# Performance work log

Hardware: AMD Instinct MI355X
Metric: run time of the kernel (lower is better)

Reference implementation:

```python
import jax, jax.numpy as jnp
import numpy as np

IN_FEATURES = 4096
OUT_FEATURES = 11008


def setup_inputs() -> dict:
    key = jax.random.key(0)
    kx, kw, ks, kb = jax.random.split(key, 4)
    x = jax.random.normal(kx, (64, IN_FEATURES), dtype=jnp.float32)
    # int8 quantized weight, stored as int32 for portability (values in [-128, 127])
    weight_quantized = jax.random.randint(kw, (OUT_FEATURES, IN_FEATURES), -128, 128, dtype=jnp.int32)
    # per-tensor scale, as produced by quantize_weights_int8: |w|.max()/127
    weight_scale = jnp.asarray(0.01, dtype=jnp.float32)
    bias = jax.random.normal(kb, (OUT_FEATURES,), dtype=jnp.float32) * 0.02
    return {"x": x, "weight_quantized": weight_quantized, "weight_scale": weight_scale, "bias": bias}


def reference(x, weight_quantized, weight_scale, bias):
    # dequantize_weights_int8: q.float() * scale, then F.linear(x, W, b) = x @ W.T + b
    weight = weight_quantized.astype(jnp.float32) * weight_scale  # [out, in]
    return jnp.einsum('mi,oi->mo', x, weight) + bias
```

## Files before the change

kernel.cpp:

```cpp
#include <hip/hip_runtime.h>
#include <hip/hip_bf16.h>


#define M_DIM 64
#define N_DIM 11008
#define K_DIM 4096
#define KSPLIT 4
#define KC (K_DIM / KSPLIT)
#define OUT_ELEMS (M_DIM * N_DIM)

typedef __attribute__((ext_vector_type(8))) short bf16x8;
typedef __attribute__((ext_vector_type(4))) float f32x4;
typedef __attribute__((ext_vector_type(4))) int i32x4;
typedef __attribute__((ext_vector_type(8))) short s16x8;

__device__ __forceinline__ short f2bf(float f) {
    unsigned int u = __builtin_bit_cast(unsigned int, f);
    u = u + 0x7FFFu + ((u >> 16) & 1u);
    return (short)(u >> 16);
}
__device__ __forceinline__ short i2bf(int q) {
    float f = (float)q;
    return (short)(__builtin_bit_cast(unsigned int, f) >> 16);
}

__global__ __launch_bounds__(256) void convert_x_kernel(const float* __restrict__ x,
                                                        short* __restrict__ xs) {
    int idx = blockIdx.x * 256 + threadIdx.x;
    const f32x4* p = (const f32x4*)x + (size_t)idx * 2;
    f32x4 a = p[0], b = p[1];
    s16x8 h;
    h[0] = f2bf(a.x); h[1] = f2bf(a.y); h[2] = f2bf(a.z); h[3] = f2bf(a.w);
    h[4] = f2bf(b.x); h[5] = f2bf(b.y); h[6] = f2bf(b.z); h[7] = f2bf(b.w);
    *((s16x8*)xs + idx) = h;
}

__global__ __launch_bounds__(64) void qgemm_kernel(const short* __restrict__ xs,
                                                   const int* __restrict__ wq,
                                                   float* __restrict__ part) {
    const int lane = threadIdx.x;
    const int quad = lane >> 4;
    const int l16  = lane & 15;
    const int n0   = blockIdx.x * 16;
    const int ks   = blockIdx.y;
    const int kc0  = ks * KC;

    const int* wrow = wq + (size_t)(n0 + l16) * K_DIM + kc0 + quad * 8;
    const short* xrow = xs + (size_t)l16 * K_DIM + kc0 + quad * 8;

    f32x4 acc[4] = {f32x4{0,0,0,0}, f32x4{0,0,0,0}, f32x4{0,0,0,0}, f32x4{0,0,0,0}};

    #pragma unroll 4
    for (int kk = 0; kk < KC; kk += 32) {
        i32x4 b0 = __builtin_nontemporal_load((const i32x4*)(wrow + kk));
        i32x4 b1 = __builtin_nontemporal_load((const i32x4*)(wrow + kk + 4));
        bf16x8 bfrag;
        bfrag[0] = i2bf(b0.x); bfrag[1] = i2bf(b0.y);
        bfrag[2] = i2bf(b0.z); bfrag[3] = i2bf(b0.w);
        bfrag[4] = i2bf(b1.x); bfrag[5] = i2bf(b1.y);
        bfrag[6] = i2bf(b1.z); bfrag[7] = i2bf(b1.w);

        #pragma unroll
        for (int mi = 0; mi < 4; ++mi) {
            bf16x8 afrag = *(const bf16x8*)(xrow + (size_t)mi * 16 * K_DIM + kk);
            acc[mi] = __builtin_amdgcn_mfma_f32_16x16x32_bf16(afrag, bfrag, acc[mi], 0, 0, 0);
        }
    }

    float* ps = part + (size_t)ks * OUT_ELEMS + n0 + l16;
    #pragma unroll
    for (int mi = 0; mi < 4; ++mi) {
        #pragma unroll
        for (int r = 0; r < 4; ++r) {
            int m = mi * 16 + quad * 4 + r;
            ps[(size_t)m * N_DIM] = acc[mi][r];
        }
    }
}

__global__ __launch_bounds__(256) void reduce_kernel(const float* __restrict__ part,
                                                     const float* __restrict__ scale_p,
                                                     const float* __restrict__ bias,
                                                     float* __restrict__ out) {
    int i4 = blockIdx.x * 256 + threadIdx.x;
    float s = *scale_p;
    int col4 = i4 % 2752;
    f32x4 b = *(const f32x4*)(bias + col4 * 4);
    f32x4 a0 = *((const f32x4*)part + i4);
    f32x4 a1 = *((const f32x4*)(part + (size_t)OUT_ELEMS) + i4);
    f32x4 a2 = *((const f32x4*)(part + (size_t)2 * OUT_ELEMS) + i4);
    f32x4 a3 = *((const f32x4*)(part + (size_t)3 * OUT_ELEMS) + i4);
    f32x4 r;
    r.x = (a0.x + a1.x + a2.x + a3.x) * s + b.x;
    r.y = (a0.y + a1.y + a2.y + a3.y) * s + b.y;
    r.z = (a0.z + a1.z + a2.z + a3.z) * s + b.z;
    r.w = (a0.w + a1.w + a2.w + a3.w) * s + b.w;
    *((f32x4*)out + i4) = r;
}

extern "C" void kernel_launch(void* const* d_in, const int* in_sizes, int n_in,
                              void* d_out, int out_size, void* d_ws, size_t ws_size,
                              hipStream_t stream) {
    const float* x     = (const float*)d_in[0];
    const int*   wq    = (const int*)d_in[1];
    const float* scale = (const float*)d_in[2];
    const float* bias  = (const float*)d_in[3];
    float* out = (float*)d_out;

    float* part = (float*)d_ws;
    short* xs   = (short*)((char*)d_ws + (size_t)KSPLIT * OUT_ELEMS * 4);

    convert_x_kernel<<<128, 256, 0, stream>>>(x, xs);

    dim3 grid(N_DIM / 16, KSPLIT);
    qgemm_kernel<<<grid, 64, 0, stream>>>(xs, wq, part);

    reduce_kernel<<<688, 256, 0, stream>>>(part, scale, bias, out);
}
```

Before: 289.6 us.

## Stage weight and activation tiles via direct global-to-LDS loads with double buffering

The GEMM is restructured into 256-thread blocks covering 64 output columns. Each block double-buffers 64-wide K tiles of int32 weights and bf16 activations into LDS using global_load_lds, with XOR swizzling to avoid bank conflicts. The next tile's loads overlap the current tile's MFMAs, and the activation tile is shared across four waves. K-split doubles to 8 for more parallelism, which also raises partial-sum traffic in the reduce kernel.

```diff
diff --git a/kernel.cpp b/kernel.cpp
--- a/kernel.cpp
+++ b/kernel.cpp
@@ -5,9 +5,15 @@
 #define M_DIM 64
 #define N_DIM 11008
 #define K_DIM 4096
-#define KSPLIT 4
+#define KSPLIT 8
 #define KC (K_DIM / KSPLIT)
+#define BK 64
+#define NIT (KC / BK)
 #define OUT_ELEMS (M_DIM * N_DIM)
+
+#define WBYTES (64 * BK * 4)
+#define XBYTES (64 * BK * 2)
+#define BUFBYTES (WBYTES + XBYTES)
 
 typedef __attribute__((ext_vector_type(8))) short bf16x8;
 typedef __attribute__((ext_vector_type(4))) float f32x4;
@@ -24,6 +30,13 @@
     return (short)(__builtin_bit_cast(unsigned int, f) >> 16);
 }
 
+__device__ __forceinline__ void gload_lds(const void* g, void* l) {
+    __builtin_amdgcn_global_load_lds(
+        (const __attribute__((address_space(1))) unsigned int*)g,
+        (__attribute__((address_space(3))) unsigned int*)l,
+        16, 0, 0);
+}
+
 __global__ __launch_bounds__(256) void convert_x_kernel(const float* __restrict__ x,
                                                         short* __restrict__ xs) {
     int idx = blockIdx.x * 256 + threadIdx.x;
@@ -35,39 +48,87 @@
     *((s16x8*)xs + idx) = h;
 }
 
-__global__ __launch_bounds__(64) void qgemm_kernel(const short* __restrict__ xs,
-                                                   const int* __restrict__ wq,
-                                                   float* __restrict__ part) {
-    const int lane = threadIdx.x;
+__global__ __launch_bounds__(256) void qgemm_kernel(const short* __restrict__ xs,
+                                                    const int* __restrict__ wq,
+                                                    float* __restrict__ part) {
+    __shared__ char smem[2 * BUFBYTES];
+
+    const int t    = threadIdx.x;
+    const int wav  = t >> 6;
+    const int lane = t & 63;
     const int quad = lane >> 4;
     const int l16  = lane & 15;
-    const int n0   = blockIdx.x * 16;
+    const int n0   = blockIdx.x * 64;
     const int ks   = blockIdx.y;
     const int kc0  = ks * KC;
 
-    const int* wrow = wq + (size_t)(n0 + l16) * K_DIM + kc0 + quad * 8;
-    const short* xrow = xs + (size_t)l16 * K_DIM + kc0 + quad * 8;
+    const int wrow4 = t >> 4;
+    const int wch   = (t & 15) ^ wrow4;
+    const int* wsrc = wq + (size_t)(n0 + wrow4) * K_DIM + kc0 + wch * 4;
+    const int xm  = t >> 3;
+    const int xch = (t & 7) ^ (xm & 7);
+    const short* xsrc = xs + (size_t)xm * K_DIM + kc0 + xch * 8;
+
+    char* const wsl = smem + t * 16;
+    char* const xsl = smem + WBYTES + t * 16;
+
+    auto stage = [&](int buf, int kb) {
+        char* wl = wsl + buf * BUFBYTES;
+        char* xl = xsl + buf * BUFBYTES;
+        #pragma unroll
+        for (int j = 0; j < 4; ++j)
+            gload_lds(wsrc + (size_t)j * 16 * K_DIM + kb, wl + j * 4096);
+        #pragma unroll
+        for (int j = 0; j < 2; ++j)
+            gload_lds(xsrc + (size_t)j * 32 * K_DIM + kb, xl + j * 4096);
+    };
 
     f32x4 acc[4] = {f32x4{0,0,0,0}, f32x4{0,0,0,0}, f32x4{0,0,0,0}, f32x4{0,0,0,0}};
 
-    #pragma unroll 4
-    for (int kk = 0; kk < KC; kk += 32) {
-        i32x4 b0 = __builtin_nontemporal_load((const i32x4*)(wrow + kk));
-        i32x4 b1 = __builtin_nontemporal_load((const i32x4*)(wrow + kk + 4));
-        bf16x8 bfrag;
-        bfrag[0] = i2bf(b0.x); bfrag[1] = i2bf(b0.y);
-        bfrag[2] = i2bf(b0.z); bfrag[3] = i2bf(b0.w);
-        bfrag[4] = i2bf(b1.x); bfrag[5] = i2bf(b1.y);
-        bfrag[6] = i2bf(b1.z); bfrag[7] = i2bf(b1.w);
+    const int wrow = wav * 16 + l16;
+
+    stage(0, 0);
+    for (int it = 0; it < NIT; ++it) {
+        if (it + 1 < NIT) {
+            stage((it + 1) & 1, (it + 1) * BK);
+            __atomic_signal_fence(__ATOMIC_SEQ_CST);
+            __builtin_amdgcn_s_waitcnt(0x0F76);
+        } else {
+            __atomic_signal_fence(__ATOMIC_SEQ_CST);
+            __builtin_amdgcn_s_waitcnt(0x0F70);
+        }
+        __builtin_amdgcn_s_barrier();
+        __atomic_signal_fence(__ATOMIC_SEQ_CST);
+
+        const int*   wl = (const int*)(smem + (it & 1) * BUFBYTES);
+        const short* xl = (const short*)(smem + (it & 1) * BUFBYTES + WBYTES);
 
         #pragma unroll
-        for (int mi = 0; mi < 4; ++mi) {
-            bf16x8 afrag = *(const bf16x8*)(xrow + (size_t)mi * 16 * K_DIM + kk);
-            acc[mi] = __builtin_amdgcn_mfma_f32_16x16x32_bf16(afrag, bfrag, acc[mi], 0, 0, 0);
+        for (int kk = 0; kk < BK; kk += 32) {
+            const int c0 = kk / 4 + quad * 2;
+            i32x4 w0 = *(const i32x4*)(wl + wrow * 64 + ((c0 ^ l16) * 4));
+            i32x4 w1 = *(const i32x4*)(wl + wrow * 64 + (((c0 + 1) ^ l16) * 4));
+            bf16x8 bfrag;
+            bfrag[0] = i2bf(w0.x); bfrag[1] = i2bf(w0.y);
+            bfrag[2] = i2bf(w0.z); bfrag[3] = i2bf(w0.w);
+            bfrag[4] = i2bf(w1.x); bfrag[5] = i2bf(w1.y);
+            bfrag[6] = i2bf(w1.z); bfrag[7] = i2bf(w1.w);
+
+            const int cx = kk / 8 + quad;
+            #pragma unroll
+            for (int mi = 0; mi < 4; ++mi) {
+                const int m = mi * 16 + l16;
+                bf16x8 afrag = *(const bf16x8*)(xl + m * 64 + ((cx ^ (l16 & 7)) * 8));
+                acc[mi] = __builtin_amdgcn_mfma_f32_16x16x32_bf16(afrag, bfrag, acc[mi], 0, 0, 0);
+            }
         }
+
+        __atomic_signal_fence(__ATOMIC_SEQ_CST);
+        __builtin_amdgcn_s_barrier();
+        __atomic_signal_fence(__ATOMIC_SEQ_CST);
     }
 
-    float* ps = part + (size_t)ks * OUT_ELEMS + n0 + l16;
+    float* ps = part + (size_t)ks * OUT_ELEMS + n0 + wav * 16 + l16;
     #pragma unroll
     for (int mi = 0; mi < 4; ++mi) {
         #pragma unroll
@@ -86,15 +147,15 @@
     float s = *scale_p;
     int col4 = i4 % 2752;
     f32x4 b = *(const f32x4*)(bias + col4 * 4);
-    f32x4 a0 = *((const f32x4*)part + i4);
-    f32x4 a1 = *((const f32x4*)(part + (size_t)OUT_ELEMS) + i4);
-    f32x4 a2 = *((const f32x4*)(part + (size_t)2 * OUT_ELEMS) + i4);
-    f32x4 a3 = *((const f32x4*)(part + (size_t)3 * OUT_ELEMS) + i4);
+    f32x4 a = *((const f32x4*)part + i4);
+    #pragma unroll
+    for (int sl = 1; sl < KSPLIT; ++sl) {
+        f32x4 c = *((const f32x4*)(part + (size_t)sl * OUT_ELEMS) + i4);
+        a.x += c.x; a.y += c.y; a.z += c.z; a.w += c.w;
+    }
     f32x4 r;
-    r.x = (a0.x + a1.x + a2.x + a3.x) * s + b.x;
-    r.y = (a0.y + a1.y + a2.y + a3.y) * s + b.y;
-    r.z = (a0.z + a1.z + a2.z + a3.z) * s + b.z;
-    r.w = (a0.w + a1.w + a2.w + a3.w) * s + b.w;
+    r.x = a.x * s + b.x; r.y = a.y * s + b.y;
+    r.z = a.z * s + b.z; r.w = a.w * s + b.w;
     *((f32x4*)out + i4) = r;
 }
 
@@ -112,8 +173,8 @@
 
     convert_x_kernel<<<128, 256, 0, stream>>>(x, xs);
 
-    dim3 grid(N_DIM / 16, KSPLIT);
-    qgemm_kernel<<<grid, 64, 0, stream>>>(xs, wq, part);
+    dim3 grid(N_DIM / 64, KSPLIT);
+    qgemm_kernel<<<grid, 256, 0, stream>>>(xs, wq, part);
 
     reduce_kernel<<<688, 256, 0, stream>>>(part, scale, bias, out);
 }
```

New measurement: 271.5 us. -6.3%, faster.

## Fuse split-K reduction into GEMM block via LDS and prefetch next K step

Applied to the files above, without the earlier changes.

Moves the four K-splits from separate blocks into four waves of one 256-thread block. Their partial sums are combined in shared memory, then scale and bias are applied before writing the output directly. This removes the partial-sum workspace round trip and the separate reduce kernel launch. It also adds software prefetching of the next iteration's weight and activation fragments to overlap loads with MFMA. The cost is a __syncthreads, extra LDS use and higher register pressure, and the output stores are now scalar with a 64-byte-wide pattern per row.

```diff
diff --git a/kernel.cpp b/kernel.cpp
--- a/kernel.cpp
+++ b/kernel.cpp
@@ -5,9 +5,7 @@
 #define M_DIM 64
 #define N_DIM 11008
 #define K_DIM 4096
-#define KSPLIT 4
-#define KC (K_DIM / KSPLIT)
-#define OUT_ELEMS (M_DIM * N_DIM)
+#define KC (K_DIM / 4)
 
 typedef __attribute__((ext_vector_type(8))) short bf16x8;
 typedef __attribute__((ext_vector_type(4))) float f32x4;
@@ -35,67 +33,77 @@
     *((s16x8*)xs + idx) = h;
 }
 
-__global__ __launch_bounds__(64) void qgemm_kernel(const short* __restrict__ xs,
-                                                   const int* __restrict__ wq,
-                                                   float* __restrict__ part) {
-    const int lane = threadIdx.x;
+__global__ __launch_bounds__(256) void qgemm_kernel(const short* __restrict__ xs,
+                                                    const int* __restrict__ wq,
+                                                    const float* __restrict__ scale_p,
+                                                    const float* __restrict__ bias,
+                                                    float* __restrict__ out) {
+    __shared__ float red[4][16][64];
+
+    const int t    = threadIdx.x;
+    const int wv   = t >> 6;
+    const int lane = t & 63;
     const int quad = lane >> 4;
     const int l16  = lane & 15;
     const int n0   = blockIdx.x * 16;
-    const int ks   = blockIdx.y;
-    const int kc0  = ks * KC;
 
-    const int* wrow = wq + (size_t)(n0 + l16) * K_DIM + kc0 + quad * 8;
-    const short* xrow = xs + (size_t)l16 * K_DIM + kc0 + quad * 8;
+    const int kbase = wv * KC;
+    const int* wp = wq + (size_t)(n0 + l16) * K_DIM + kbase + quad * 8;
+    const short* xp = xs + (size_t)l16 * K_DIM + kbase + quad * 8;
 
     f32x4 acc[4] = {f32x4{0,0,0,0}, f32x4{0,0,0,0}, f32x4{0,0,0,0}, f32x4{0,0,0,0}};
 
-    #pragma unroll 4
+    i32x4 w0 = __builtin_nontemporal_load((const i32x4*)(wp));
+    i32x4 w1 = __builtin_nontemporal_load((const i32x4*)(wp + 4));
+    bf16x8 af[4];
+    #pragma unroll
+    for (int mi = 0; mi < 4; ++mi)
+        af[mi] = *(const bf16x8*)(xp + (size_t)mi * 16 * K_DIM);
+
     for (int kk = 0; kk < KC; kk += 32) {
-        i32x4 b0 = __builtin_nontemporal_load((const i32x4*)(wrow + kk));
-        i32x4 b1 = __builtin_nontemporal_load((const i32x4*)(wrow + kk + 4));
+        const int nk = (kk + 32 < KC) ? (kk + 32) : kk;
+        i32x4 nw0 = __builtin_nontemporal_load((const i32x4*)(wp + nk));
+        i32x4 nw1 = __builtin_nontemporal_load((const i32x4*)(wp + nk + 4));
+        bf16x8 naf[4];
+        #pragma unroll
+        for (int mi = 0; mi < 4; ++mi)
+            naf[mi] = *(const bf16x8*)(xp + (size_t)mi * 16 * K_DIM + nk);
+
         bf16x8 bfrag;
-        bfrag[0] = i2bf(b0.x); bfrag[1] = i2bf(b0.y);
-        bfrag[2] = i2bf(b0.z); bfrag[3] = i2bf(b0.w);
-        bfrag[4] = i2bf(b1.x); bfrag[5] = i2bf(b1.y);
-        bfrag[6] = i2bf(b1.z); bfrag[7] = i2bf(b1.w);
+        bfrag[0] = i2bf(w0.x); bfrag[1] = i2bf(w0.y);
+        bfrag[2] = i2bf(w0.z); bfrag[3] = i2bf(w0.w);
+        bfrag[4] = i2bf(w1.x); bfrag[5] = i2bf(w1.y);
+        bfrag[6] = i2bf(w1.z); bfrag[7] = i2bf(w1.w);
 
         #pragma unroll
-        for (int mi = 0; mi < 4; ++mi) {
-            bf16x8 afrag = *(const bf16x8*)(xrow + (size_t)mi * 16 * K_DIM + kk);
-            acc[mi] = __builtin_amdgcn_mfma_f32_16x16x32_bf16(afrag, bfrag, acc[mi], 0, 0, 0);
+        for (int mi = 0; mi < 4; ++mi)
+            acc[mi] = __builtin_amdgcn_mfma_f32_16x16x32_bf16(af[mi], bfrag, acc[mi], 0, 0, 0);
+
+        w0 = nw0; w1 = nw1;
+        #pragma unroll
+        for (int mi = 0; mi < 4; ++mi) af[mi] = naf[mi];
+    }
+
+    #pragma unroll
+    for (int mi = 0; mi < 4; ++mi)
+        *(f32x4*)&red[wv][l16][mi * 16 + quad * 4] = acc[mi];
+    __syncthreads();
+
+    {
+        const int n  = t & 15;
+        const int mg = t >> 4;
+        f32x4 s0 = *(const f32x4*)&red[0][n][mg * 4];
+        f32x4 s1 = *(const f32x4*)&red[1][n][mg * 4];
+        f32x4 s2 = *(const f32x4*)&red[2][n][mg * 4];
+        f32x4 s3 = *(const f32x4*)&red[3][n][mg * 4];
+        const float sc = *scale_p;
+        const float b  = bias[n0 + n];
+        #pragma unroll
+        for (int j = 0; j < 4; ++j) {
+            float v = (s0[j] + s1[j] + s2[j] + s3[j]) * sc + b;
+            out[(size_t)(mg * 4 + j) * N_DIM + n0 + n] = v;
         }
     }
-
-    float* ps = part + (size_t)ks * OUT_ELEMS + n0 + l16;
-    #pragma unroll
-    for (int mi = 0; mi < 4; ++mi) {
-        #pragma unroll
-        for (int r = 0; r < 4; ++r) {
-            int m = mi * 16 + quad * 4 + r;
-            ps[(size_t)m * N_DIM] = acc[mi][r];
-        }
-    }
-}
-
-__global__ __launch_bounds__(256) void reduce_kernel(const float* __restrict__ part,
-                                                     const float* __restrict__ scale_p,
-                                                     const float* __restrict__ bias,
-                                                     float* __restrict__ out) {
-    int i4 = blockIdx.x * 256 + threadIdx.x;
-    float s = *scale_p;
-    int col4 = i4 % 2752;
-    f32x4 b = *(const f32x4*)(bias + col4 * 4);
-    f32x4 a0 = *((const f32x4*)part + i4);
-    f32x4 a1 = *((const f32x4*)(part + (size_t)OUT_ELEMS) + i4);
-    f32x4 a2 = *((const f32x4*)(part + (size_t)2 * OUT_ELEMS) + i4);
-    f32x4 a3 = *((const f32x4*)(part + (size_t)3 * OUT_ELEMS) + i4);
-    f32x4 r;
-    r.x = (a0.x + a1.x + a2.x + a3.x) * s + b.x;
-    r.y = (a0.y + a1.y + a2.y + a3.y) * s + b.y;
-    r.z = (a0.z + a1.z + a2.z + a3.z) * s + b.z;
-    r.w = (a0.w + a1.w + a2.w + a3.w) * s + b.w;
-    *((f32x4*)out + i4) = r;
 }
 
 extern "C" void kernel_launch(void* const* d_in, const int* in_sizes, int n_in,
@@ -107,13 +115,8 @@
     const float* bias  = (const float*)d_in[3];
     float* out = (float*)d_out;
 
-    float* part = (float*)d_ws;
-    short* xs   = (short*)((char*)d_ws + (size_t)KSPLIT * OUT_ELEMS * 4);
+    short* xs = (short*)d_ws;
 
     convert_x_kernel<<<128, 256, 0, stream>>>(x, xs);
-
-    dim3 grid(N_DIM / 16, KSPLIT);
-    qgemm_kernel<<<grid, 64, 0, stream>>>(xs, wq, part);
-
-    reduce_kernel<<<688, 256, 0, stream>>>(part, scale, bias, out);
+    qgemm_kernel<<<N_DIM / 16, 256, 0, stream>>>(xs, wq, scale, bias, out);
 }
```

Measured after the change: 290.7 us. Within noise of the previous version (+0.4%).

## Stage weight tiles into LDS with async global_load_lds and split K across waves

Applied to the files above, without the earlier changes.

The qgemm kernel now uses 256-thread blocks. Each block bulk-loads its 16x1024 int32 weight slice into padded LDS with global_load_lds, then each of four waves computes a quarter of the K chunk from LDS. Partial accumulators are reduced across the waves through shared memory before being written out. This aims to issue fully coalesced, deep weight streaming in place of per-lane strided nontemporal loads, at the cost of about 66 KB of LDS per block, lower occupancy, and no overlap between the load and compute phases.

```diff
diff --git a/kernel.cpp b/kernel.cpp
--- a/kernel.cpp
+++ b/kernel.cpp
@@ -8,6 +8,7 @@
 #define KSPLIT 4
 #define KC (K_DIM / KSPLIT)
 #define OUT_ELEMS (M_DIM * N_DIM)
+#define ROWB 4112
 
 typedef __attribute__((ext_vector_type(8))) short bf16x8;
 typedef __attribute__((ext_vector_type(4))) float f32x4;
@@ -23,6 +24,19 @@
     float f = (float)q;
     return (short)(__builtin_bit_cast(unsigned int, f) >> 16);
 }
+__device__ __forceinline__ bf16x8 cvt_w(i32x4 a, i32x4 b) {
+    bf16x8 r;
+    r[0] = i2bf(a.x); r[1] = i2bf(a.y); r[2] = i2bf(a.z); r[3] = i2bf(a.w);
+    r[4] = i2bf(b.x); r[5] = i2bf(b.y); r[6] = i2bf(b.z); r[7] = i2bf(b.w);
+    return r;
+}
+
+__device__ __forceinline__ void gload_lds(const void* g, void* l) {
+    __builtin_amdgcn_global_load_lds(
+        (const __attribute__((address_space(1))) unsigned int*)g,
+        (__attribute__((address_space(3))) unsigned int*)l,
+        16, 0, 0);
+}
 
 __global__ __launch_bounds__(256) void convert_x_kernel(const float* __restrict__ x,
                                                         short* __restrict__ xs) {
@@ -35,46 +49,69 @@
     *((s16x8*)xs + idx) = h;
 }
 
-__global__ __launch_bounds__(64) void qgemm_kernel(const short* __restrict__ xs,
-                                                   const int* __restrict__ wq,
-                                                   float* __restrict__ part) {
-    const int lane = threadIdx.x;
+__global__ __launch_bounds__(256) void qgemm_kernel(const short* __restrict__ xs,
+                                                    const int* __restrict__ wq,
+                                                    float* __restrict__ part) {
+    __shared__ __align__(16) char smem[16 * ROWB];
+
+    const int t    = threadIdx.x;
+    const int wv   = t >> 6;
+    const int lane = t & 63;
     const int quad = lane >> 4;
     const int l16  = lane & 15;
     const int n0   = blockIdx.x * 16;
     const int ks   = blockIdx.y;
-    const int kc0  = ks * KC;
+    const int k0   = ks * KC;
 
-    const int* wrow = wq + (size_t)(n0 + l16) * K_DIM + kc0 + quad * 8;
-    const short* xrow = xs + (size_t)l16 * K_DIM + kc0 + quad * 8;
+    {
+        #pragma unroll
+        for (int rr = 0; rr < 4; ++rr) {
+            const int r = wv * 4 + rr;
+            const int* src = wq + (size_t)(n0 + r) * K_DIM + k0 + lane * 4;
+            char* dst = smem + r * ROWB + lane * 16;
+            #pragma unroll
+            for (int i = 0; i < 4; ++i)
+                gload_lds(src + i * 256, dst + i * 1024);
+        }
+    }
+    __syncthreads();
 
     f32x4 acc[4] = {f32x4{0,0,0,0}, f32x4{0,0,0,0}, f32x4{0,0,0,0}, f32x4{0,0,0,0}};
 
-    #pragma unroll 4
-    for (int kk = 0; kk < KC; kk += 32) {
-        i32x4 b0 = __builtin_nontemporal_load((const i32x4*)(wrow + kk));
-        i32x4 b1 = __builtin_nontemporal_load((const i32x4*)(wrow + kk + 4));
-        bf16x8 bfrag;
-        bfrag[0] = i2bf(b0.x); bfrag[1] = i2bf(b0.y);
-        bfrag[2] = i2bf(b0.z); bfrag[3] = i2bf(b0.w);
-        bfrag[4] = i2bf(b1.x); bfrag[5] = i2bf(b1.y);
-        bfrag[6] = i2bf(b1.z); bfrag[7] = i2bf(b1.w);
+    const char* wrow = smem + l16 * ROWB;
+    const int   ko   = wv * 256 + quad * 8;
+    const short* xp  = xs + (size_t)l16 * K_DIM + k0 + ko;
 
+    #pragma unroll
+    for (int kk = 0; kk < 256; kk += 32) {
+        i32x4 w0 = *(const i32x4*)(wrow + (ko + kk) * 4);
+        i32x4 w1 = *(const i32x4*)(wrow + (ko + kk + 4) * 4);
+        bf16x8 bfrag = cvt_w(w0, w1);
         #pragma unroll
         for (int mi = 0; mi < 4; ++mi) {
-            bf16x8 afrag = *(const bf16x8*)(xrow + (size_t)mi * 16 * K_DIM + kk);
+            bf16x8 afrag = *(const bf16x8*)(xp + (size_t)mi * 16 * K_DIM + kk);
             acc[mi] = __builtin_amdgcn_mfma_f32_16x16x32_bf16(afrag, bfrag, acc[mi], 0, 0, 0);
         }
     }
+    __syncthreads();
 
-    float* ps = part + (size_t)ks * OUT_ELEMS + n0 + l16;
+    float (*red)[16][64] = (float (*)[16][64])smem;
     #pragma unroll
-    for (int mi = 0; mi < 4; ++mi) {
+    for (int mi = 0; mi < 4; ++mi)
+        *(f32x4*)&red[wv][l16][mi * 16 + quad * 4] = acc[mi];
+    __syncthreads();
+
+    {
+        const int n  = t & 15;
+        const int mg = t >> 4;
+        f32x4 s0 = *(const f32x4*)&red[0][n][mg * 4];
+        f32x4 s1 = *(const f32x4*)&red[1][n][mg * 4];
+        f32x4 s2 = *(const f32x4*)&red[2][n][mg * 4];
+        f32x4 s3 = *(const f32x4*)&red[3][n][mg * 4];
+        float* ps = part + (size_t)ks * OUT_ELEMS + n0 + n;
         #pragma unroll
-        for (int r = 0; r < 4; ++r) {
-            int m = mi * 16 + quad * 4 + r;
-            ps[(size_t)m * N_DIM] = acc[mi][r];
-        }
+        for (int j = 0; j < 4; ++j)
+            ps[(size_t)(mg * 4 + j) * N_DIM] = s0[j] + s1[j] + s2[j] + s3[j];
     }
 }
 
@@ -86,15 +123,15 @@
     float s = *scale_p;
     int col4 = i4 % 2752;
     f32x4 b = *(const f32x4*)(bias + col4 * 4);
-    f32x4 a0 = *((const f32x4*)part + i4);
-    f32x4 a1 = *((const f32x4*)(part + (size_t)OUT_ELEMS) + i4);
-    f32x4 a2 = *((const f32x4*)(part + (size_t)2 * OUT_ELEMS) + i4);
-    f32x4 a3 = *((const f32x4*)(part + (size_t)3 * OUT_ELEMS) + i4);
+    f32x4 a = *((const f32x4*)part + i4);
+    #pragma unroll
+    for (int sl = 1; sl < KSPLIT; ++sl) {
+        f32x4 c = *((const f32x4*)(part + (size_t)sl * OUT_ELEMS) + i4);
+        a.x += c.x; a.y += c.y; a.z += c.z; a.w += c.w;
+    }
     f32x4 r;
-    r.x = (a0.x + a1.x + a2.x + a3.x) * s + b.x;
-    r.y = (a0.y + a1.y + a2.y + a3.y) * s + b.y;
-    r.z = (a0.z + a1.z + a2.z + a3.z) * s + b.z;
-    r.w = (a0.w + a1.w + a2.w + a3.w) * s + b.w;
+    r.x = a.x * s + b.x; r.y = a.y * s + b.y;
+    r.z = a.z * s + b.z; r.w = a.w * s + b.w;
     *((f32x4*)out + i4) = r;
 }
 
@@ -113,7 +150,7 @@
     convert_x_kernel<<<128, 256, 0, stream>>>(x, xs);
 
     dim3 grid(N_DIM / 16, KSPLIT);
-    qgemm_kernel<<<grid, 64, 0, stream>>>(xs, wq, part);
+    qgemm_kernel<<<grid, 256, 0, stream>>>(xs, wq, part);
 
     reduce_kernel<<<688, 256, 0, stream>>>(part, scale, bias, out);
 }
```

Measured after the change: 281.2 us. 2.9% less time.
